# Kernel optimization log

Hardware: AMD Instinct MI355X
Metric: run time of the kernel (lower is better)

## Reference

```python
import jax, jax.numpy as jnp
import numpy as np

HEAD_DIM = 64
SCALE = HEAD_DIM ** -0.5
NUM_HEADS = 16


def setup_inputs() -> dict:
    key = jax.random.key(0)
    k1, k2, k3, k4 = jax.random.split(key, 4)
    dim = 1024
    query = jax.random.normal(k1, (8, 512, dim), dtype=jnp.float32)
    memory = jax.random.normal(k2, (8, 512, dim), dtype=jnp.float32)
    # nn.Linear weights are [out, in]; scale like default init
    W_Q = jax.random.normal(k3, (dim, dim), dtype=jnp.float32) * (dim ** -0.5)
    W_K = jax.random.normal(k4, (dim, dim), dtype=jnp.float32) * (dim ** -0.5)
    return {"query": query, "memory": memory, "W_Q": W_Q, "W_K": W_K}


def reference(query, memory, W_Q, W_K):
    # Q: [K, Lq, E], K: [B, Lk, E]  (E = H * D)
    Q = query @ W_Q.T
    Km = memory @ W_K.T
    Kb, Lq, E = Q.shape
    Bb, Lk, _ = Km.shape
    Qh = Q.reshape(Kb, Lq, NUM_HEADS, HEAD_DIM).transpose(0, 2, 1, 3)  # K H q D
    Kh = Km.reshape(Bb, Lk, NUM_HEADS, HEAD_DIM).transpose(0, 2, 1, 3)  # B H k D
    # logits: [B, K, H, q, k]
    logits = jnp.einsum('ahqd,bhkd->bahqk', Qh, Kh) * SCALE
    energies = jax.nn.logsumexp(logits, axis=-2) / SCALE  # [B, K, H, k]
    energies = energies.mean(axis=1)  # [B, H, k]
    return energies
```

## Files before the change

kernel.cpp:

```cpp
#include <hip/hip_runtime.h>
#include <hip/hip_bf16.h>

typedef short short8 __attribute__((ext_vector_type(8)));
typedef float f32x4 __attribute__((ext_vector_type(4)));
typedef unsigned short u16;

__device__ __forceinline__ unsigned short f2bf(float f) {
  unsigned int u = __float_as_uint(f);
  u += 0x7fffu + ((u >> 16) & 1u);
  return (unsigned short)(u >> 16);
}

__device__ __forceinline__ void glds16(const void* g, void* l) {
  __builtin_amdgcn_global_load_lds(
      (const __attribute__((address_space(1))) unsigned int*)g,
      (__attribute__((address_space(3))) unsigned int*)l, 16, 0, 0);
}

__device__ __forceinline__ void drain_then_sync() {
  __builtin_amdgcn_s_waitcnt(0);
  __syncthreads();
}

__global__ __launch_bounds__(256) void prep(const float4* __restrict__ q,
                                            const float4* __restrict__ m,
                                            const float4* __restrict__ wq,
                                            const float4* __restrict__ wk,
                                            ushort4* __restrict__ qb,
                                            ushort4* __restrict__ mb,
                                            ushort4* __restrict__ wqb,
                                            ushort4* __restrict__ wkb,
                                            float4* __restrict__ out0) {
  const int i = blockIdx.x * 256 + threadIdx.x;
  const float c = 0.18033688011112042f;
  if (i < 1048576) {
    float4 v = q[i];
    ushort4 o; o.x = f2bf(v.x); o.y = f2bf(v.y); o.z = f2bf(v.z); o.w = f2bf(v.w);
    qb[i] = o;
  } else if (i < 2097152) {
    float4 v = m[i - 1048576];
    ushort4 o; o.x = f2bf(v.x); o.y = f2bf(v.y); o.z = f2bf(v.z); o.w = f2bf(v.w);
    mb[i - 1048576] = o;
  } else if (i < 2359296) {
    float4 v = wq[i - 2097152];
    ushort4 o; o.x = f2bf(v.x * c); o.y = f2bf(v.y * c); o.z = f2bf(v.z * c); o.w = f2bf(v.w * c);
    wqb[i - 2097152] = o;
  } else if (i < 2621440) {
    float4 v = wk[i - 2359296];
    ushort4 o; o.x = f2bf(v.x); o.y = f2bf(v.y); o.z = f2bf(v.z); o.w = f2bf(v.w);
    wkb[i - 2359296] = o;
  } else if (i < 2637824) {
    out0[i - 2621440] = (float4){0.f, 0.f, 0.f, 0.f};
  }
}

__global__ __launch_bounds__(512) void gemm_db(const u16* __restrict__ A0,
                                               const u16* __restrict__ B0,
                                               u16* __restrict__ C0,
                                               const u16* __restrict__ A1,
                                               const u16* __restrict__ B1,
                                               u16* __restrict__ C1) {
  __shared__ u16 As[2][128 * 64];
  __shared__ u16 Bs[2][128 * 64];
  const int zz = blockIdx.x & 1;
  const u16* A = zz ? A1 : A0;
  const u16* B = zz ? B1 : B0;
  u16* C = zz ? C1 : C0;
  const int t = threadIdx.x;
  const int lane = t & 63, wave = t >> 6;
  const int l15 = lane & 15, quad = lane >> 4;
  const int mb = (blockIdx.x >> 1) * 128;
  const int nb = blockIdx.y * 128;
  const int wm = (wave & 1) * 64;
  const int wn = (wave >> 1) * 32;

  const int srow = lane >> 3;
  const int scol = ((lane & 7) ^ srow) * 8;
  const int sw = l15 & 7;

  f32x4 acc[4][2];
#pragma unroll
  for (int i = 0; i < 4; i++)
#pragma unroll
    for (int j = 0; j < 2; j++) acc[i][j] = (f32x4){0.f, 0.f, 0.f, 0.f};

#pragma unroll
  for (int j = 0; j < 2; j++) {
    const int g = wave * 2 + j;
    glds16(A + (size_t)(mb + g * 8 + srow) * 1024 + scol, &As[0][g * 512 + lane * 8]);
    glds16(B + (size_t)(nb + g * 8 + srow) * 1024 + scol, &Bs[0][g * 512 + lane * 8]);
  }

  for (int it = 0; it < 16; ++it) {
    drain_then_sync();
    if (it < 15) {
      const int kb = (it + 1) * 64, bf_ = (it + 1) & 1;
#pragma unroll
      for (int j = 0; j < 2; j++) {
        const int g = wave * 2 + j;
        glds16(A + (size_t)(mb + g * 8 + srow) * 1024 + kb + scol, &As[bf_][g * 512 + lane * 8]);
        glds16(B + (size_t)(nb + g * 8 + srow) * 1024 + kb + scol, &Bs[bf_][g * 512 + lane * 8]);
      }
    }
    const u16* as = As[it & 1];
    const u16* bs = Bs[it & 1];
#pragma unroll
    for (int kk = 0; kk < 2; kk++) {
      const int cb = kk * 4;
      short8 af[4], bfr[2];
#pragma unroll
      for (int mi = 0; mi < 4; mi++)
        af[mi] = *(const short8*)&as[(wm + mi * 16 + l15) * 64 + ((cb + quad) ^ sw) * 8];
#pragma unroll
      for (int ni = 0; ni < 2; ni++)
        bfr[ni] = *(const short8*)&bs[(wn + ni * 16 + l15) * 64 + ((cb + quad) ^ sw) * 8];
#pragma unroll
      for (int mi = 0; mi < 4; mi++)
#pragma unroll
        for (int ni = 0; ni < 2; ni++)
          acc[mi][ni] = __builtin_amdgcn_mfma_f32_16x16x32_bf16(
              af[mi], bfr[ni], acc[mi][ni], 0, 0, 0);
    }
  }

#pragma unroll
  for (int mi = 0; mi < 4; mi++)
#pragma unroll
    for (int r = 0; r < 4; r++) {
      const int row = mb + wm + mi * 16 + quad * 4 + r;
      const size_t base = (size_t)row * 1024 + nb + wn;
#pragma unroll
      for (int ni = 0; ni < 2; ni++)
        C[base + ni * 16 + l15] = f2bf(acc[mi][ni][r]);
    }
}

__global__ __launch_bounds__(256) void attn_lse5(const u16* __restrict__ Qp,
                                                 const u16* __restrict__ Kp,
                                                 float* __restrict__ out) {
  __shared__ u16 qs[2][128 * 64];
  const int t = threadIdx.x;
  const int lane = t & 63, wave = t >> 6;
  const int l15 = lane & 15, quad = lane >> 4;
  const int kt = blockIdx.x & 1, aa = blockIdx.x >> 1;
  const int h = blockIdx.y, b = blockIdx.z;
  const int kwave = kt * 256 + wave * 64;

  short8 klo[4], khi[4];
#pragma unroll
  for (int tt = 0; tt < 4; tt++) {
    const short8* kg = (const short8*)(Kp + (size_t)(b * 512 + kwave + tt * 16 + l15) * 1024
                                       + h * 64 + quad * 8);
    klo[tt] = kg[0];
    khi[tt] = kg[4];
  }

  const int srow = lane >> 3;
  const int scol = ((lane & 7) ^ srow) * 8;
  const u16* qbase = Qp + (size_t)(aa * 512) * 1024 + h * 64;

  const int sw = l15 & 7;
  const int colLo = (quad ^ sw) * 8;
  const int colHi = ((4 + quad) ^ sw) * 8;
  const int rrow = l15 * 64;

  const f32x4 z4 = (f32x4){0.f, 0.f, 0.f, 0.f};
  float cs0 = 0.f, cs1 = 0.f, cs2 = 0.f, cs3 = 0.f;

#pragma unroll
  for (int j = 0; j < 4; j++) {
    const int g = wave * 4 + j;
    glds16(qbase + (size_t)(g * 8 + srow) * 1024 + scol, &qs[0][g * 512 + lane * 8]);
  }

  for (int i = 0; i < 4; i++) {
    drain_then_sync();
    if (i < 3) {
#pragma unroll
      for (int j = 0; j < 4; j++) {
        const int g = wave * 4 + j;
        glds16(qbase + (size_t)((i + 1) * 128 + g * 8 + srow) * 1024 + scol,
               &qs[(i + 1) & 1][g * 512 + lane * 8]);
      }
    }
    const u16* buf = qs[i & 1];
#pragma unroll
    for (int qt = 0; qt < 8; qt++) {
      short8 alo = *(const short8*)&buf[qt * 1024 + rrow + colLo];
      short8 ahi = *(const short8*)&buf[qt * 1024 + rrow + colHi];
      f32x4 a0 = __builtin_amdgcn_mfma_f32_16x16x32_bf16(
          ahi, khi[0], __builtin_amdgcn_mfma_f32_16x16x32_bf16(alo, klo[0], z4, 0, 0, 0), 0, 0, 0);
      f32x4 a1 = __builtin_amdgcn_mfma_f32_16x16x32_bf16(
          ahi, khi[1], __builtin_amdgcn_mfma_f32_16x16x32_bf16(alo, klo[1], z4, 0, 0, 0), 0, 0, 0);
      f32x4 a2 = __builtin_amdgcn_mfma_f32_16x16x32_bf16(
          ahi, khi[2], __builtin_amdgcn_mfma_f32_16x16x32_bf16(alo, klo[2], z4, 0, 0, 0), 0, 0, 0);
      f32x4 a3 = __builtin_amdgcn_mfma_f32_16x16x32_bf16(
          ahi, khi[3], __builtin_amdgcn_mfma_f32_16x16x32_bf16(alo, klo[3], z4, 0, 0, 0), 0, 0, 0);
#pragma unroll
      for (int r = 0; r < 4; r++) {
        cs0 += __builtin_amdgcn_exp2f(a0[r]);
        cs1 += __builtin_amdgcn_exp2f(a1[r]);
        cs2 += __builtin_amdgcn_exp2f(a2[r]);
        cs3 += __builtin_amdgcn_exp2f(a3[r]);
      }
    }
  }
  cs0 += __shfl_xor(cs0, 16); cs0 += __shfl_xor(cs0, 32);
  cs1 += __shfl_xor(cs1, 16); cs1 += __shfl_xor(cs1, 32);
  cs2 += __shfl_xor(cs2, 16); cs2 += __shfl_xor(cs2, 32);
  cs3 += __shfl_xor(cs3, 16); cs3 += __shfl_xor(cs3, 32);
  const float v = quad == 0 ? cs0 : quad == 1 ? cs1 : quad == 2 ? cs2 : cs3;
  atomicAdd(out + (size_t)b * 8192 + h * 512 + kwave + quad * 16 + l15, __logf(v));
}

extern "C" void kernel_launch(void* const* d_in, const int* in_sizes, int n_in,
                              void* d_out, int out_size, void* d_ws, size_t ws_size,
                              hipStream_t stream) {
  const float* query  = (const float*)d_in[0];
  const float* memory = (const float*)d_in[1];
  const float* wq     = (const float*)d_in[2];
  const float* wk     = (const float*)d_in[3];
  float* out = (float*)d_out;

  char* ws = (char*)d_ws;
  const size_t MB = 1024 * 1024;
  u16* qb  = (u16*)(ws);
  u16* mb_ = (u16*)(ws + 8  * MB);
  u16* wqb = (u16*)(ws + 16 * MB);
  u16* wkb = (u16*)(ws + 18 * MB);
  u16* Qp  = (u16*)(ws + 20 * MB);
  u16* Kp  = (u16*)(ws + 28 * MB);

  prep<<<10304, 256, 0, stream>>>((const float4*)query, (const float4*)memory,
                                  (const float4*)wq, (const float4*)wk,
                                  (ushort4*)qb, (ushort4*)mb_, (ushort4*)wqb,
                                  (ushort4*)wkb, (float4*)d_out);
  gemm_db<<<dim3(64, 8), 512, 0, stream>>>(qb, wqb, Qp, mb_, wkb, Kp);
  attn_lse5<<<dim3(16, 16, 8), 256, 0, stream>>>(Qp, Kp, out);
}
```

Before: 147.7 us.

## Fuse fp32-to-bf16 conversion into GEMM tile loads and drop prep kernel

Removes the separate prep kernel that converted query, memory and the weights to bf16 buffers in workspace. The projection GEMM now reads fp32 directly, scales W_Q, converts to bf16 in registers, and stores into swizzled LDS double buffers. Zeroing of the output also moves into this kernel. This saves a launch and a full read/write pass over the inputs, in exchange for twice the global read bytes per tile, register-staged prefetch instead of direct-to-LDS loads, and round-half-up rather than round-to-nearest-even conversion.

```diff
diff --git a/kernel.cpp b/kernel.cpp
--- a/kernel.cpp
+++ b/kernel.cpp
@@ -4,12 +4,7 @@
 typedef short short8 __attribute__((ext_vector_type(8)));
 typedef float f32x4 __attribute__((ext_vector_type(4)));
 typedef unsigned short u16;
-
-__device__ __forceinline__ unsigned short f2bf(float f) {
-  unsigned int u = __float_as_uint(f);
-  u += 0x7fffu + ((u >> 16) & 1u);
-  return (unsigned short)(u >> 16);
-}
+typedef unsigned int u32;
 
 __device__ __forceinline__ void glds16(const void* g, void* l) {
   __builtin_amdgcn_global_load_lds(
@@ -22,50 +17,26 @@
   __syncthreads();
 }
 
-__global__ __launch_bounds__(256) void prep(const float4* __restrict__ q,
-                                            const float4* __restrict__ m,
-                                            const float4* __restrict__ wq,
-                                            const float4* __restrict__ wk,
-                                            ushort4* __restrict__ qb,
-                                            ushort4* __restrict__ mb,
-                                            ushort4* __restrict__ wqb,
-                                            ushort4* __restrict__ wkb,
-                                            float4* __restrict__ out0) {
-  const int i = blockIdx.x * 256 + threadIdx.x;
-  const float c = 0.18033688011112042f;
-  if (i < 1048576) {
-    float4 v = q[i];
-    ushort4 o; o.x = f2bf(v.x); o.y = f2bf(v.y); o.z = f2bf(v.z); o.w = f2bf(v.w);
-    qb[i] = o;
-  } else if (i < 2097152) {
-    float4 v = m[i - 1048576];
-    ushort4 o; o.x = f2bf(v.x); o.y = f2bf(v.y); o.z = f2bf(v.z); o.w = f2bf(v.w);
-    mb[i - 1048576] = o;
-  } else if (i < 2359296) {
-    float4 v = wq[i - 2097152];
-    ushort4 o; o.x = f2bf(v.x * c); o.y = f2bf(v.y * c); o.z = f2bf(v.z * c); o.w = f2bf(v.w * c);
-    wqb[i - 2097152] = o;
-  } else if (i < 2621440) {
-    float4 v = wk[i - 2359296];
-    ushort4 o; o.x = f2bf(v.x); o.y = f2bf(v.y); o.z = f2bf(v.z); o.w = f2bf(v.w);
-    wkb[i - 2359296] = o;
-  } else if (i < 2637824) {
-    out0[i - 2621440] = (float4){0.f, 0.f, 0.f, 0.f};
-  }
-}
-
-__global__ __launch_bounds__(512) void gemm_db(const u16* __restrict__ A0,
-                                               const u16* __restrict__ B0,
-                                               u16* __restrict__ C0,
-                                               const u16* __restrict__ A1,
-                                               const u16* __restrict__ B1,
-                                               u16* __restrict__ C1) {
+__device__ __forceinline__ u32 pack_bf(float f0, float f1) {
+  u32 u0 = __float_as_uint(f0) + 0x8000u;
+  u32 u1 = __float_as_uint(f1) + 0x8000u;
+  return (u0 >> 16) | (u1 & 0xffff0000u);
+}
+
+__global__ __launch_bounds__(512) void gemm_f32(const float* __restrict__ Aq,
+                                                const float* __restrict__ Bq,
+                                                u16* __restrict__ Cq,
+                                                const float* __restrict__ Ak,
+                                                const float* __restrict__ Bk,
+                                                u16* __restrict__ Ck,
+                                                float4* __restrict__ out4) {
   __shared__ u16 As[2][128 * 64];
   __shared__ u16 Bs[2][128 * 64];
   const int zz = blockIdx.x & 1;
-  const u16* A = zz ? A1 : A0;
-  const u16* B = zz ? B1 : B0;
-  u16* C = zz ? C1 : C0;
+  const float* A32 = zz ? Ak : Aq;
+  const float* B32 = zz ? Bk : Bq;
+  u16* C = zz ? Ck : Cq;
+  const float bscale = zz ? 1.0f : 0.18033688011112042f;
   const int t = threadIdx.x;
   const int lane = t & 63, wave = t >> 6;
   const int l15 = lane & 15, quad = lane >> 4;
@@ -73,34 +44,59 @@
   const int nb = blockIdx.y * 128;
   const int wm = (wave & 1) * 64;
   const int wn = (wave >> 1) * 32;
-
-  const int srow = lane >> 3;
-  const int scol = ((lane & 7) ^ srow) * 8;
   const int sw = l15 & 7;
 
+  if (blockIdx.y == 0 && (blockIdx.x >> 1) < 8 && !zz) {
+    const int zi = ((blockIdx.x >> 1) * 512 + t) * 4;
+    out4[zi] = (float4){0.f, 0.f, 0.f, 0.f};
+    out4[zi + 1] = (float4){0.f, 0.f, 0.f, 0.f};
+    out4[zi + 2] = (float4){0.f, 0.f, 0.f, 0.f};
+    out4[zi + 3] = (float4){0.f, 0.f, 0.f, 0.f};
+  }
+
+  const int srow2 = t >> 2;
+  const int cg = t & 3;
+  const int sw8 = srow2 & 7;
+  const int c0 = (cg * 2) ^ sw8, c1 = (cg * 2 + 1) ^ sw8;
+  const int wofs0 = srow2 * 64 + c0 * 8;
+  const int wofs1 = srow2 * 64 + c1 * 8;
+  const float* gA = A32 + (size_t)(mb + srow2) * 1024 + cg * 16;
+  const float* gB = B32 + (size_t)(nb + srow2) * 1024 + cg * 16;
+
   f32x4 acc[4][2];
 #pragma unroll
   for (int i = 0; i < 4; i++)
 #pragma unroll
     for (int j = 0; j < 2; j++) acc[i][j] = (f32x4){0.f, 0.f, 0.f, 0.f};
 
-#pragma unroll
-  for (int j = 0; j < 2; j++) {
-    const int g = wave * 2 + j;
-    glds16(A + (size_t)(mb + g * 8 + srow) * 1024 + scol, &As[0][g * 512 + lane * 8]);
-    glds16(B + (size_t)(nb + g * 8 + srow) * 1024 + scol, &Bs[0][g * 512 + lane * 8]);
+  {
+    const float4* a4 = (const float4*)gA;
+    const float4* b4 = (const float4*)gB;
+    float4 a0 = a4[0], a1 = a4[1], a2 = a4[2], a3 = a4[3];
+    float4 b0 = b4[0], b1 = b4[1], b2 = b4[2], b3 = b4[3];
+    b0.x *= bscale; b0.y *= bscale; b0.z *= bscale; b0.w *= bscale;
+    b1.x *= bscale; b1.y *= bscale; b1.z *= bscale; b1.w *= bscale;
+    b2.x *= bscale; b2.y *= bscale; b2.z *= bscale; b2.w *= bscale;
+    b3.x *= bscale; b3.y *= bscale; b3.z *= bscale; b3.w *= bscale;
+    uint4 pa0 = {pack_bf(a0.x, a0.y), pack_bf(a0.z, a0.w), pack_bf(a1.x, a1.y), pack_bf(a1.z, a1.w)};
+    uint4 pa1 = {pack_bf(a2.x, a2.y), pack_bf(a2.z, a2.w), pack_bf(a3.x, a3.y), pack_bf(a3.z, a3.w)};
+    uint4 pb0 = {pack_bf(b0.x, b0.y), pack_bf(b0.z, b0.w), pack_bf(b1.x, b1.y), pack_bf(b1.z, b1.w)};
+    uint4 pb1 = {pack_bf(b2.x, b2.y), pack_bf(b2.z, b2.w), pack_bf(b3.x, b3.y), pack_bf(b3.z, b3.w)};
+    *(uint4*)&As[0][wofs0] = pa0;
+    *(uint4*)&As[0][wofs1] = pa1;
+    *(uint4*)&Bs[0][wofs0] = pb0;
+    *(uint4*)&Bs[0][wofs1] = pb1;
   }
 
   for (int it = 0; it < 16; ++it) {
     drain_then_sync();
+    float4 a0, a1, a2, a3, b0, b1, b2, b3;
     if (it < 15) {
-      const int kb = (it + 1) * 64, bf_ = (it + 1) & 1;
-#pragma unroll
-      for (int j = 0; j < 2; j++) {
-        const int g = wave * 2 + j;
-        glds16(A + (size_t)(mb + g * 8 + srow) * 1024 + kb + scol, &As[bf_][g * 512 + lane * 8]);
-        glds16(B + (size_t)(nb + g * 8 + srow) * 1024 + kb + scol, &Bs[bf_][g * 512 + lane * 8]);
-      }
+      const int kb = (it + 1) * 64;
+      const float4* a4 = (const float4*)(gA + kb);
+      const float4* b4 = (const float4*)(gB + kb);
+      a0 = a4[0]; a1 = a4[1]; a2 = a4[2]; a3 = a4[3];
+      b0 = b4[0]; b1 = b4[1]; b2 = b4[2]; b3 = b4[3];
     }
     const u16* as = As[it & 1];
     const u16* bs = Bs[it & 1];
@@ -121,6 +117,21 @@
           acc[mi][ni] = __builtin_amdgcn_mfma_f32_16x16x32_bf16(
               af[mi], bfr[ni], acc[mi][ni], 0, 0, 0);
     }
+    if (it < 15) {
+      const int nbuf = (it + 1) & 1;
+      b0.x *= bscale; b0.y *= bscale; b0.z *= bscale; b0.w *= bscale;
+      b1.x *= bscale; b1.y *= bscale; b1.z *= bscale; b1.w *= bscale;
+      b2.x *= bscale; b2.y *= bscale; b2.z *= bscale; b2.w *= bscale;
+      b3.x *= bscale; b3.y *= bscale; b3.z *= bscale; b3.w *= bscale;
+      uint4 pa0 = {pack_bf(a0.x, a0.y), pack_bf(a0.z, a0.w), pack_bf(a1.x, a1.y), pack_bf(a1.z, a1.w)};
+      uint4 pa1 = {pack_bf(a2.x, a2.y), pack_bf(a2.z, a2.w), pack_bf(a3.x, a3.y), pack_bf(a3.z, a3.w)};
+      uint4 pb0 = {pack_bf(b0.x, b0.y), pack_bf(b0.z, b0.w), pack_bf(b1.x, b1.y), pack_bf(b1.z, b1.w)};
+      uint4 pb1 = {pack_bf(b2.x, b2.y), pack_bf(b2.z, b2.w), pack_bf(b3.x, b3.y), pack_bf(b3.z, b3.w)};
+      *(uint4*)&As[nbuf][wofs0] = pa0;
+      *(uint4*)&As[nbuf][wofs1] = pa1;
+      *(uint4*)&Bs[nbuf][wofs0] = pb0;
+      *(uint4*)&Bs[nbuf][wofs1] = pb1;
+    }
   }
 
 #pragma unroll
@@ -130,8 +141,12 @@
       const int row = mb + wm + mi * 16 + quad * 4 + r;
       const size_t base = (size_t)row * 1024 + nb + wn;
 #pragma unroll
-      for (int ni = 0; ni < 2; ni++)
-        C[base + ni * 16 + l15] = f2bf(acc[mi][ni][r]);
+      for (int ni = 0; ni < 2; ni++) {
+        const float v = acc[mi][ni][r];
+        u32 u = __float_as_uint(v);
+        u += 0x7fffu + ((u >> 16) & 1u);
+        C[base + ni * 16 + l15] = (u16)(u >> 16);
+      }
     }
 }
 
@@ -224,17 +239,10 @@
 
   char* ws = (char*)d_ws;
   const size_t MB = 1024 * 1024;
-  u16* qb  = (u16*)(ws);
-  u16* mb_ = (u16*)(ws + 8  * MB);
-  u16* wqb = (u16*)(ws + 16 * MB);
-  u16* wkb = (u16*)(ws + 18 * MB);
-  u16* Qp  = (u16*)(ws + 20 * MB);
-  u16* Kp  = (u16*)(ws + 28 * MB);
-
-  prep<<<10304, 256, 0, stream>>>((const float4*)query, (const float4*)memory,
-                                  (const float4*)wq, (const float4*)wk,
-                                  (ushort4*)qb, (ushort4*)mb_, (ushort4*)wqb,
-                                  (ushort4*)wkb, (float4*)d_out);
-  gemm_db<<<dim3(64, 8), 512, 0, stream>>>(qb, wqb, Qp, mb_, wkb, Kp);
+  u16* Qp = (u16*)(ws);
+  u16* Kp = (u16*)(ws + 8 * MB);
+
+  gemm_f32<<<dim3(64, 8), 512, 0, stream>>>(query, wq, Qp, memory, wk, Kp,
+                                            (float4*)out);
   attn_lse5<<<dim3(16, 16, 8), 256, 0, stream>>>(Qp, Kp, out);
 }
```

Result: slower. 161.3 us (+9.3%).

## Split attention over query chunks with partial exp-sum buffer and separate log reduction

Applied to the files above, without the earlier changes.

Splits each attention block's 512 query rows into four 128-row chunks handled by separate blocks, which multiplies the grid by four. Blocks atomically add raw exp-sums into a per-(b,h,k,aa) buffer, and a new reduction kernel takes logs and sums over the 8 query batches. The aim is more parallelism and occupancy, and dropping the double-buffered LDS loop. The cost is four times the K-fragment loads, more atomics, one extra kernel launch, and a larger zero-fill in prep.

```diff
diff --git a/kernel.cpp b/kernel.cpp
--- a/kernel.cpp
+++ b/kernel.cpp
@@ -30,7 +30,7 @@
                                             ushort4* __restrict__ mb,
                                             ushort4* __restrict__ wqb,
                                             ushort4* __restrict__ wkb,
-                                            float4* __restrict__ out0) {
+                                            float4* __restrict__ buf4) {
   const int i = blockIdx.x * 256 + threadIdx.x;
   const float c = 0.18033688011112042f;
   if (i < 1048576) {
@@ -49,8 +49,8 @@
     float4 v = wk[i - 2359296];
     ushort4 o; o.x = f2bf(v.x); o.y = f2bf(v.y); o.z = f2bf(v.z); o.w = f2bf(v.w);
     wkb[i - 2359296] = o;
-  } else if (i < 2637824) {
-    out0[i - 2621440] = (float4){0.f, 0.f, 0.f, 0.f};
+  } else if (i < 2752512) {
+    buf4[i - 2621440] = (float4){0.f, 0.f, 0.f, 0.f};
   }
 }
 
@@ -135,14 +135,16 @@
     }
 }
 
-__global__ __launch_bounds__(256) void attn_lse5(const u16* __restrict__ Qp,
-                                                 const u16* __restrict__ Kp,
-                                                 float* __restrict__ out) {
-  __shared__ u16 qs[2][128 * 64];
+__global__ __launch_bounds__(256) void attn_ps(const u16* __restrict__ Qp,
+                                               const u16* __restrict__ Kp,
+                                               float* __restrict__ buf) {
+  __shared__ u16 qs[128 * 64];
   const int t = threadIdx.x;
   const int lane = t & 63, wave = t >> 6;
   const int l15 = lane & 15, quad = lane >> 4;
-  const int kt = blockIdx.x & 1, aa = blockIdx.x >> 1;
+  const int aa = blockIdx.x & 7;
+  const int kt = (blockIdx.x >> 3) & 1;
+  const int qsplit = blockIdx.x >> 4;
   const int h = blockIdx.y, b = blockIdx.z;
   const int kwave = kt * 256 + wave * 64;
 
@@ -157,7 +159,13 @@
 
   const int srow = lane >> 3;
   const int scol = ((lane & 7) ^ srow) * 8;
-  const u16* qbase = Qp + (size_t)(aa * 512) * 1024 + h * 64;
+  const u16* qbase = Qp + (size_t)(aa * 512 + qsplit * 128) * 1024 + h * 64;
+
+#pragma unroll
+  for (int j = 0; j < 4; j++) {
+    const int g = wave * 4 + j;
+    glds16(qbase + (size_t)(g * 8 + srow) * 1024 + scol, &qs[g * 512 + lane * 8]);
+  }
 
   const int sw = l15 & 7;
   const int colLo = (quad ^ sw) * 8;
@@ -167,42 +175,26 @@
   const f32x4 z4 = (f32x4){0.f, 0.f, 0.f, 0.f};
   float cs0 = 0.f, cs1 = 0.f, cs2 = 0.f, cs3 = 0.f;
 
-#pragma unroll
-  for (int j = 0; j < 4; j++) {
-    const int g = wave * 4 + j;
-    glds16(qbase + (size_t)(g * 8 + srow) * 1024 + scol, &qs[0][g * 512 + lane * 8]);
-  }
-
-  for (int i = 0; i < 4; i++) {
-    drain_then_sync();
-    if (i < 3) {
-#pragma unroll
-      for (int j = 0; j < 4; j++) {
-        const int g = wave * 4 + j;
-        glds16(qbase + (size_t)((i + 1) * 128 + g * 8 + srow) * 1024 + scol,
-               &qs[(i + 1) & 1][g * 512 + lane * 8]);
-      }
-    }
-    const u16* buf = qs[i & 1];
-#pragma unroll
-    for (int qt = 0; qt < 8; qt++) {
-      short8 alo = *(const short8*)&buf[qt * 1024 + rrow + colLo];
-      short8 ahi = *(const short8*)&buf[qt * 1024 + rrow + colHi];
-      f32x4 a0 = __builtin_amdgcn_mfma_f32_16x16x32_bf16(
-          ahi, khi[0], __builtin_amdgcn_mfma_f32_16x16x32_bf16(alo, klo[0], z4, 0, 0, 0), 0, 0, 0);
-      f32x4 a1 = __builtin_amdgcn_mfma_f32_16x16x32_bf16(
-          ahi, khi[1], __builtin_amdgcn_mfma_f32_16x16x32_bf16(alo, klo[1], z4, 0, 0, 0), 0, 0, 0);
-      f32x4 a2 = __builtin_amdgcn_mfma_f32_16x16x32_bf16(
-          ahi, khi[2], __builtin_amdgcn_mfma_f32_16x16x32_bf16(alo, klo[2], z4, 0, 0, 0), 0, 0, 0);
-      f32x4 a3 = __builtin_amdgcn_mfma_f32_16x16x32_bf16(
-          ahi, khi[3], __builtin_amdgcn_mfma_f32_16x16x32_bf16(alo, klo[3], z4, 0, 0, 0), 0, 0, 0);
-#pragma unroll
-      for (int r = 0; r < 4; r++) {
-        cs0 += __builtin_amdgcn_exp2f(a0[r]);
-        cs1 += __builtin_amdgcn_exp2f(a1[r]);
-        cs2 += __builtin_amdgcn_exp2f(a2[r]);
-        cs3 += __builtin_amdgcn_exp2f(a3[r]);
-      }
+  drain_then_sync();
+
+#pragma unroll
+  for (int qt = 0; qt < 8; qt++) {
+    short8 alo = *(const short8*)&qs[qt * 1024 + rrow + colLo];
+    short8 ahi = *(const short8*)&qs[qt * 1024 + rrow + colHi];
+    f32x4 a0 = __builtin_amdgcn_mfma_f32_16x16x32_bf16(
+        ahi, khi[0], __builtin_amdgcn_mfma_f32_16x16x32_bf16(alo, klo[0], z4, 0, 0, 0), 0, 0, 0);
+    f32x4 a1 = __builtin_amdgcn_mfma_f32_16x16x32_bf16(
+        ahi, khi[1], __builtin_amdgcn_mfma_f32_16x16x32_bf16(alo, klo[1], z4, 0, 0, 0), 0, 0, 0);
+    f32x4 a2 = __builtin_amdgcn_mfma_f32_16x16x32_bf16(
+        ahi, khi[2], __builtin_amdgcn_mfma_f32_16x16x32_bf16(alo, klo[2], z4, 0, 0, 0), 0, 0, 0);
+    f32x4 a3 = __builtin_amdgcn_mfma_f32_16x16x32_bf16(
+        ahi, khi[3], __builtin_amdgcn_mfma_f32_16x16x32_bf16(alo, klo[3], z4, 0, 0, 0), 0, 0, 0);
+#pragma unroll
+    for (int r = 0; r < 4; r++) {
+      cs0 += __builtin_amdgcn_exp2f(a0[r]);
+      cs1 += __builtin_amdgcn_exp2f(a1[r]);
+      cs2 += __builtin_amdgcn_exp2f(a2[r]);
+      cs3 += __builtin_amdgcn_exp2f(a3[r]);
     }
   }
   cs0 += __shfl_xor(cs0, 16); cs0 += __shfl_xor(cs0, 32);
@@ -210,7 +202,17 @@
   cs2 += __shfl_xor(cs2, 16); cs2 += __shfl_xor(cs2, 32);
   cs3 += __shfl_xor(cs3, 16); cs3 += __shfl_xor(cs3, 32);
   const float v = quad == 0 ? cs0 : quad == 1 ? cs1 : quad == 2 ? cs2 : cs3;
-  atomicAdd(out + (size_t)b * 8192 + h * 512 + kwave + quad * 16 + l15, __logf(v));
+  const size_t k = (size_t)(b * 16 + h) * 512 + kwave + quad * 16 + l15;
+  atomicAdd(buf + k * 8 + aa, v);
+}
+
+__global__ __launch_bounds__(256) void lse_reduce(const float* __restrict__ buf,
+                                                  float* __restrict__ out) {
+  const int i = blockIdx.x * 256 + threadIdx.x;
+  const float4* p = (const float4*)(buf + (size_t)i * 8);
+  float4 x = p[0], y = p[1];
+  out[i] = __logf(x.x) + __logf(x.y) + __logf(x.z) + __logf(x.w)
+         + __logf(y.x) + __logf(y.y) + __logf(y.z) + __logf(y.w);
 }
 
 extern "C" void kernel_launch(void* const* d_in, const int* in_sizes, int n_in,
@@ -224,17 +226,19 @@
 
   char* ws = (char*)d_ws;
   const size_t MB = 1024 * 1024;
-  u16* qb  = (u16*)(ws);
-  u16* mb_ = (u16*)(ws + 8  * MB);
-  u16* wqb = (u16*)(ws + 16 * MB);
-  u16* wkb = (u16*)(ws + 18 * MB);
-  u16* Qp  = (u16*)(ws + 20 * MB);
-  u16* Kp  = (u16*)(ws + 28 * MB);
-
-  prep<<<10304, 256, 0, stream>>>((const float4*)query, (const float4*)memory,
+  u16* qb   = (u16*)(ws);
+  u16* mb_  = (u16*)(ws + 8  * MB);
+  u16* wqb  = (u16*)(ws + 16 * MB);
+  u16* wkb  = (u16*)(ws + 18 * MB);
+  u16* Qp   = (u16*)(ws + 20 * MB);
+  u16* Kp   = (u16*)(ws + 28 * MB);
+  float* buf = (float*)(ws + 36 * MB);
+
+  prep<<<10752, 256, 0, stream>>>((const float4*)query, (const float4*)memory,
                                   (const float4*)wq, (const float4*)wk,
                                   (ushort4*)qb, (ushort4*)mb_, (ushort4*)wqb,
-                                  (ushort4*)wkb, (float4*)d_out);
+                                  (ushort4*)wkb, (float4*)buf);
   gemm_db<<<dim3(64, 8), 512, 0, stream>>>(qb, wqb, Qp, mb_, wkb, Kp);
-  attn_lse5<<<dim3(16, 16, 8), 256, 0, stream>>>(Qp, Kp, out);
-}
+  attn_ps<<<dim3(64, 16, 8), 256, 0, stream>>>(Qp, Kp, buf);
+  lse_reduce<<<256, 256, 0, stream>>>(buf, out);
+}
```

Result: slower. 163.4 us (+10.7%).
